# Kernel optimization log

Measured on AMD Instinct MI355X. Metric: run time of the kernel, lower is better.

## Reference

```python
import jax, jax.numpy as jnp
import numpy as np

EMB = 64
L = 2
NU = 100000
NI = 50000
ER = 1000000
ET = 800000
EP = 200000


def setup_inputs() -> dict:
    key = jax.random.key(0)
    ks = jax.random.split(key, 32)
    f = jnp.float32
    def nrm(k, shape, s=0.01):
        return (jax.random.normal(k, shape) * s).astype(f)
    inp = {}
    # graph structure (int)
    inp['rate_src'] = jax.random.randint(ks[0], (ER,), 0, NU)
    inp['rate_dst'] = jax.random.randint(ks[1], (ER,), 0, NI)
    inp['trust_src'] = jax.random.randint(ks[2], (ET,), 0, NU)
    inp['trust_dst'] = jax.random.randint(ks[3], (ET,), 0, NU)
    inp['pos_u'] = jax.random.randint(ks[4], (EP,), 0, NU)
    inp['pos_i'] = jax.random.randint(ks[5], (EP,), 0, NI)
    inp['neg_u'] = jax.random.randint(ks[6], (EP,), 0, NU)
    inp['neg_i'] = jax.random.randint(ks[7], (EP,), 0, NI)
    # embeddings (init normal(0, 0.01) per init_weights)
    inp['eu'] = nrm(ks[8], (NU, EMB))
    inp['ei'] = nrm(ks[9], (NI, EMB))
    # per-rel GATv2 params, stacked over L layers; [:,0]=fc_src, [:,1]=fc_dst
    inp['rate_W'] = nrm(ks[10], (L, 2, EMB, EMB))
    inp['rate_b'] = jnp.zeros((L, 2, EMB), f)
    inp['rate_attn'] = nrm(ks[11], (L, EMB), 0.1)
    inp['rate_bias'] = jnp.zeros((L, EMB), f)
    inp['rb_W'] = nrm(ks[12], (L, 2, EMB, EMB))
    inp['rb_b'] = jnp.zeros((L, 2, EMB), f)
    inp['rb_attn'] = nrm(ks[13], (L, EMB), 0.1)
    inp['rb_bias'] = jnp.zeros((L, EMB), f)
    inp['tr_W'] = nrm(ks[14], (L, 2, EMB, EMB))
    inp['tr_b'] = jnp.zeros((L, 2, EMB), f)
    inp['tr_attn'] = nrm(ks[15], (L, EMB), 0.1)
    inp['tr_bias'] = jnp.zeros((L, EMB), f)
    # attention-gate MLPs: [:, 0]=influence, [:, 1]=interest
    inp['attW1'] = nrm(ks[16], (L, 2, 2 * EMB, 2 * EMB))
    inp['attb1'] = jnp.zeros((L, 2, 2 * EMB), f)
    inp['attW2'] = nrm(ks[17], (L, 2, 2 * EMB))
    inp['attb2'] = jnp.zeros((L, 2), f)
    return inp


def gatv2(hs, hd, src, dst, Ws, bs, Wd, bd, attn, bias, n_dst):
    # DGL GATv2Conv, num_heads=1: e = attn . leaky_relu(Ws h_u + Wd h_v), slope 0.2
    fs = hs @ Ws + bs          # [Ns, E]
    fd = hd @ Wd + bd          # [Nd, E]
    e = jax.nn.leaky_relu(fs[src] + fd[dst], 0.2) @ attn  # [E]
    m = jax.ops.segment_max(e, dst, num_segments=n_dst)
    ex = jnp.exp(e - m[dst])
    denom = jax.ops.segment_sum(ex, dst, num_segments=n_dst)
    alpha = ex / denom[dst]
    out = jax.ops.segment_sum(alpha[:, None] * fs[src], dst, num_segments=n_dst)
    return out + bias


def _bn1(x):
    # BatchNorm1d(1), training-mode batch stats, affine identity at init
    mu = jnp.mean(x)
    var = jnp.mean((x - mu) ** 2)
    return (x - mu) * jax.lax.rsqrt(var + 1e-5)


def reference(eu, ei, rate_W, rate_b, rate_attn, rate_bias, rb_W, rb_b, rb_attn,
              rb_bias, tr_W, tr_b, tr_attn, tr_bias, attW1, attb1, attW2, attb2,
              rate_src, rate_dst, trust_src, trust_dst, pos_u, pos_i, neg_u, neg_i):
    n_users, n_items = eu.shape[0], ei.shape[0]
    hu, hi = eu, ei
    res_u, res_i = [eu], [ei]
    for l in range(rate_W.shape[0]):
        # interest diffusion: rate (user->item) and rated-by (item->user, reverse edges)
        hi_new = gatv2(hu, hi, rate_src, rate_dst, rate_W[l, 0], rate_b[l, 0],
                       rate_W[l, 1], rate_b[l, 1], rate_attn[l], rate_bias[l], n_items) + hi
        q = gatv2(hi, hu, rate_dst, rate_src, rb_W[l, 0], rb_b[l, 0],
                  rb_W[l, 1], rb_b[l, 1], rb_attn[l], rb_bias[l], n_users)
        # influence diffusion: trust (user->user)
        p = gatv2(hu, hu, trust_src, trust_dst, tr_W[l, 0], tr_b[l, 0],
                  tr_W[l, 1], tr_b[l, 1], tr_attn[l], tr_bias[l], n_users)
        def att(h2, i):
            z = (h2 @ attW1[l, i] + attb1[l, i]) @ attW2[l, i] + attb2[l, i]  # [N]
            return jax.nn.leaky_relu(_bn1(z), 0.01)
        a_inf = att(jnp.concatenate([hu, p], axis=1), 0)
        a_int = att(jnp.concatenate([hu, q], axis=1), 1)
        gamma = jax.nn.softmax(jnp.stack([a_inf, a_int], axis=1), axis=1)  # [N,2]
        hu = gamma[:, 0:1] * p + gamma[:, 1:2] * q + hu
        hi = hi_new
        res_u.append(hu)
        res_i.append(hi)
    hu_all = jnp.concatenate(res_u, axis=1)  # [NU, EMB*(1+L)]
    hi_all = jnp.concatenate(res_i, axis=1)
    pos = jnp.sum(hu_all[pos_u] * hi_all[pos_i], axis=1, keepdims=True)  # [EP,1]
    neg = jnp.sum(hu_all[neg_u] * hi_all[neg_i], axis=1, keepdims=True)
    return pos, neg
```

## Files before the change

### kernel.cpp

```cpp
#include <hip/hip_runtime.h>
#include <hip/hip_bf16.h>
#include <hip/hip_fp16.h>
#include <cstdint>

typedef __hip_bfloat16 bf16;
typedef __attribute__((ext_vector_type(8))) short frag_ab;
typedef __attribute__((ext_vector_type(4))) float frag_cd;
typedef __attribute__((ext_vector_type(4))) short short4v;
typedef __attribute__((ext_vector_type(8))) short short8v;
typedef unsigned short u16;

#define CAPA 56
#define CAPB 40
#define CAPC 32

__device__ __forceinline__ float b2f(short s){
  return __uint_as_float(((unsigned)(unsigned short)s) << 16);
}
__device__ __forceinline__ float h2f(short s){
  __half h; __builtin_memcpy(&h, &s, 2); return __half2float(h);
}
__device__ __forceinline__ short f2h_s(float x){
  __half h = __float2half(x);
  short s; __builtin_memcpy(&s, &h, 2); return s;
}
__device__ __forceinline__ void bf_split(float x, short& hi, short& lo){
  bf16 h = __float2bfloat16(x);
  float hf = __bfloat162float(h);
  bf16 l = __float2bfloat16(x - hf);
  __builtin_memcpy(&hi, &h, 2);
  __builtin_memcpy(&lo, &l, 2);
}

__device__ __forceinline__ float wave_sum(float v){
#pragma unroll
  for (int o = 32; o > 0; o >>= 1) v += __shfl_down(v, o, 64);
  return v;
}

__global__ void k_wsplit(const float* __restrict__ rateW, const float* __restrict__ rbW,
                         const float* __restrict__ trW,
                         short* __restrict__ Whi, short* __restrict__ Wlo){
  int tid = blockIdx.x * 256 + threadIdx.x;
  if (tid >= 12 * 4096) return;
  int m = tid >> 12, rem = tid & 4095;
  int lane = rem >> 6, rem2 = rem & 63;
  int pair = rem2 >> 3, j = rem2 & 7;
  int c = pair >> 1, h = pair & 1;
  int rel = m >> 2, li = m & 3;
  const float* base = (rel == 0) ? rateW : (rel == 1) ? rbW : trW;
  float v = base[(size_t)li * 4096 + (32 * h + (lane >> 4) * 8 + j) * 64 + 16 * c + (lane & 15)];
  short sh, sl; bf_split(v, sh, sl);
  Whi[tid] = sh; Wlo[tid] = sl;
}

__device__ __forceinline__ void dev_linear(int rowb, int nloc, int gofs, int nglob,
    const float* __restrict__ x, int xs, int xo,
    const short* __restrict__ Whi, const short* __restrict__ Wlo, int mcount,
    int m0, int m1, int m2, int m3,
    const float* b0, const float* b1, const float* b2, const float* b3,
    bf16* o0, bf16* o1, bf16* o2, bf16* o3){
  int lane = threadIdx.x & 63, w = threadIdx.x >> 6;
  int quad = lane >> 4, n16 = lane & 15;
  int rowbase = rowb + w * 16;
  if (rowbase >= nloc) return;
  int lrow = rowbase + n16; if (lrow >= nloc) lrow = nloc - 1;
  const float* xp = x + (size_t)lrow * xs + xo;
  frag_ab ahi[2], alo[2];
#pragma unroll
  for (int h = 0; h < 2; ++h){
    frag_ab vh, vl;
#pragma unroll
    for (int j = 0; j < 8; ++j){
      float xv = xp[32 * h + quad * 8 + j];
      short sh, sl; bf_split(xv, sh, sl);
      vh[j] = sh; vl[j] = sl;
    }
    ahi[h] = vh; alo[h] = vl;
  }
  int ms[4] = {m0, m1, m2, m3};
  const float* bs[4] = {b0, b1, b2, b3};
  bf16* os[4] = {o0, o1, o2, o3};
  for (int i = 0; i < mcount; ++i){
    const frag_ab* Bh = (const frag_ab*)(Whi + (size_t)ms[i] * 4096 + lane * 64);
    const frag_ab* Bl = (const frag_ab*)(Wlo + (size_t)ms[i] * 4096 + lane * 64);
    frag_cd acc[4];
#pragma unroll
    for (int c = 0; c < 4; ++c) acc[c] = frag_cd{0.f, 0.f, 0.f, 0.f};
#pragma unroll
    for (int c = 0; c < 4; ++c)
#pragma unroll
      for (int h = 0; h < 2; ++h){
        frag_ab bh = Bh[c * 2 + h], bl = Bl[c * 2 + h];
        acc[c] = __builtin_amdgcn_mfma_f32_16x16x32_bf16(ahi[h], bh, acc[c], 0, 0, 0);
        acc[c] = __builtin_amdgcn_mfma_f32_16x16x32_bf16(alo[h], bh, acc[c], 0, 0, 0);
        acc[c] = __builtin_amdgcn_mfma_f32_16x16x32_bf16(ahi[h], bl, acc[c], 0, 0, 0);
      }
    const float* bb = bs[i];
    bf16* oo = os[i];
#pragma unroll
    for (int reg = 0; reg < 4; ++reg){
      int r = rowbase + quad * 4 + reg;
      if (r >= nloc || gofs + r >= nglob) continue;
#pragma unroll
      for (int c = 0; c < 4; ++c)
        oo[(size_t)(gofs + r) * 64 + 16 * c + n16] = __float2bfloat16(acc[c][reg] + bb[16 * c + n16]);
    }
  }
}

struct LinArgs {
  int nblk; const float* x; int xs, xo, n, mcount;
  int m0, m1, m2, m3;
  const float *b0, *b1, *b2, *b3;
  bf16 *o0, *o1, *o2, *o3;
};
struct PrepArgs {
  int NBH, ER, ET;
  const int *rate_src, *rate_dst, *trust_dst;
  int *cntA, *cntB, *cntC;
  u16 *posA, *posB, *posC;
  const short *Whi, *Wlo;
  LinArgs LU, LI;
  const float *W1, *b1v, *W2, *b2v;
  float *vvec, *cs;
};

__global__ void k_prep(PrepArgs a){
  int b = blockIdx.x, t = threadIdx.x;
  if (b < a.NBH){
    int k = b * 256 + t;
    if (k < a.ER){
      int d = a.rate_dst[k], s = a.rate_src[k];
      a.posA[k] = (u16)atomicAdd(a.cntA + d, 1);
      a.posB[k] = (u16)atomicAdd(a.cntB + s, 1);
    }
    if (k < a.ET){
      a.posC[k] = (u16)atomicAdd(a.cntC + a.trust_dst[k], 1);
    }
    return;
  }
  b -= a.NBH;
  if (b < a.LU.nblk){
    dev_linear(b * 64, a.LU.n, 0, a.LU.n, a.LU.x, a.LU.xs, a.LU.xo, a.Whi, a.Wlo,
               a.LU.mcount, a.LU.m0, a.LU.m1, a.LU.m2, a.LU.m3,
               a.LU.b0, a.LU.b1, a.LU.b2, a.LU.b3, a.LU.o0, a.LU.o1, a.LU.o2, a.LU.o3);
    return;
  }
  b -= a.LU.nblk;
  if (b < a.LI.nblk){
    dev_linear(b * 64, a.LI.n, 0, a.LI.n, a.LI.x, a.LI.xs, a.LI.xo, a.Whi, a.Wlo,
               a.LI.mcount, a.LI.m0, a.LI.m1, a.LI.m2, a.LI.m3,
               a.LI.b0, a.LI.b1, a.LI.b2, a.LI.b3, a.LI.o0, a.LI.o1, a.LI.o2, a.LI.o3);
    return;
  }
  for (int it = t; it < 512; it += 256){
    int li = it >> 7, r = it & 127;
    float acc = 0.f;
    for (int c = 0; c < 128; ++c)
      acc += a.W1[(size_t)(li * 128 + r) * 128 + c] * a.W2[li * 128 + c];
    a.vvec[li * 128 + r] = acc;
    if (r == 0){
      float cacc = a.b2v[li];
      for (int c = 0; c < 128; ++c)
        cacc += a.b1v[li * 128 + c] * a.W2[li * 128 + c];
      a.cs[li] = cacc;
    }
  }
}

__global__ void k_fill(const int* __restrict__ rs_, const int* __restrict__ rd_,
                       const int* __restrict__ ts_, const int* __restrict__ td_,
                       const u16* __restrict__ posA, const u16* __restrict__ posB,
                       const u16* __restrict__ posC,
                       int* __restrict__ csrA, u16* __restrict__ csrB,
                       int* __restrict__ csrC, int ER, int ET){
  int k = blockIdx.x * 256 + threadIdx.x;
  if (k < ER){
    int s = rs_[k], d = rd_[k];
    int pa = posA[k], pb = posB[k];
    if (pa < CAPA) csrA[(size_t)d * CAPA + pa] = s;
    if (pb < CAPB) csrB[(size_t)s * CAPB + pb] = (u16)d;
  }
  if (k < ET){
    int pc = posC[k];
    if (pc < CAPC) csrC[(size_t)td_[k] * CAPC + pc] = ts_[k];
  }
}

struct GatArgs {
  int nblk, n, of16;
  const int *cnt;
  const int *csr; const u16 *csr16;
  const bf16 *fs, *fd;
  const float *attn, *bias;
  void *out; int os, oo;
  const float *res; int rs, ro;
};

template<int CAP>
__device__ __forceinline__ void dev_gat(int lb, const GatArgs& g){
  int d = lb * 4 + (threadIdx.x >> 6);
  if (d >= g.n) return;
  int lane = threadIdx.x & 63;
  int gg = lane >> 3, l8 = lane & 7;
  int c = g.cnt[d]; if (c > CAP) c = CAP;
  size_t base = (size_t)d * CAP;
  int my_s = 0;
  if (lane < c) my_s = g.csr16 ? (int)g.csr16[base + lane] : g.csr[base + lane];
  short8v dv = *(const short8v*)(g.fd + (size_t)d * 64 + 8 * l8);
  float fdv[8];
#pragma unroll
  for (int j = 0; j < 8; ++j) fdv[j] = b2f(dv[j]);
  float4 a0 = *(const float4*)(g.attn + 8 * l8);
  float4 a1 = *(const float4*)(g.attn + 8 * l8 + 4);
  float a8[8] = {a0.x, a0.y, a0.z, a0.w, a1.x, a1.y, a1.z, a1.w};
  float acc[8];
#pragma unroll
  for (int j = 0; j < 8; ++j) acc[j] = 0.f;
  float den = 0.f;
  short8v s0, s1;
  {
    int e = gg;
    int ss = __shfl(my_s, (e < c) ? e : 0, 64);
    s0 = *(const short8v*)(g.fs + (size_t)ss * 64 + 8 * l8);
  }
  s1 = s0;
  if (8 < c){
    int e = 8 + gg;
    int ss = __shfl(my_s, (e < c) ? e : 8, 64);
    s1 = *(const short8v*)(g.fs + (size_t)ss * 64 + 8 * l8);
  }
  for (int idx = 0; idx < c; idx += 8){
    short8v cur = s0;
    s0 = s1;
    int nn = idx + 16;
    if (nn < c){
      int e = nn + gg;
      int ss = __shfl(my_s, (e < c) ? e : nn, 64);
      s1 = *(const short8v*)(g.fs + (size_t)ss * 64 + 8 * l8);
    }
    bool valid = (idx + gg) < c;
    float f[8];
    float tt = 0.f;
#pragma unroll
    for (int j = 0; j < 8; ++j){
      f[j] = b2f(cur[j]);
      float v = f[j] + fdv[j];
      v = (v > 0.f) ? v : 0.2f * v;
      tt += v * a8[j];
    }
#pragma unroll
    for (int o = 1; o < 8; o <<= 1) tt += __shfl_xor(tt, o, 64);
    float ex = valid ? __expf(tt) : 0.f;
#pragma unroll
    for (int j = 0; j < 8; ++j) acc[j] += ex * f[j];
    den += ex;
  }
#pragma unroll
  for (int o = 8; o < 64; o <<= 1){
#pragma unroll
    for (int j = 0; j < 8; ++j) acc[j] += __shfl_xor(acc[j], o, 64);
    den += __shfl_xor(den, o, 64);
  }
  if (gg == 0){
    float inv = (den > 0.f) ? 1.f / den : 0.f;
    float4 b0 = *(const float4*)(g.bias + 8 * l8);
    float4 b1 = *(const float4*)(g.bias + 8 * l8 + 4);
    float o8[8];
    o8[0] = acc[0] * inv + b0.x; o8[1] = acc[1] * inv + b0.y;
    o8[2] = acc[2] * inv + b0.z; o8[3] = acc[3] * inv + b0.w;
    o8[4] = acc[4] * inv + b1.x; o8[5] = acc[5] * inv + b1.y;
    o8[6] = acc[6] * inv + b1.z; o8[7] = acc[7] * inv + b1.w;
    if (g.res){
      float4 r0 = *(const float4*)(g.res + (size_t)d * g.rs + g.ro + 8 * l8);
      float4 r1 = *(const float4*)(g.res + (size_t)d * g.rs + g.ro + 8 * l8 + 4);
      o8[0] += r0.x; o8[1] += r0.y; o8[2] += r0.z; o8[3] += r0.w;
      o8[4] += r1.x; o8[5] += r1.y; o8[6] += r1.z; o8[7] += r1.w;
    }
    if (g.of16){
      short8v hv;
#pragma unroll
      for (int j = 0; j < 8; ++j) hv[j] = f2h_s(o8[j]);
      *(short8v*)((short*)g.out + (size_t)d * g.os + g.oo + 8 * l8) = hv;
    } else {
      float* op = (float*)g.out + (size_t)d * g.os + g.oo + 8 * l8;
      *(float4*)op = make_float4(o8[0], o8[1], o8[2], o8[3]);
      *(float4*)(op + 4) = make_float4(o8[4], o8[5], o8[6], o8[7]);
    }
  }
}

template<int CA, int CB, int CC>
__global__ void k_gat3(GatArgs A, GatArgs B, GatArgs C){
  int b = blockIdx.x;
  if (b < A.nblk){ dev_gat<CA>(b, A); return; }
  b -= A.nblk;
  if (b < B.nblk){ dev_gat<CB>(b, B); return; }
  b -= B.nblk;
  dev_gat<CC>(b, C);
}

struct GzArgs {
  int nbz, NU, l;
  const float* hptr;
  const float* pf32;
  const __half* pf16;
  const __half* q;
  const float *vvec, *cs;
  float *z1, *z2, *bsums;
  const short *Whi, *Wlo;
  LinArgs LI;
};

__global__ void k_gatez(GzArgs a){
  int b = blockIdx.x;
  if (b < a.LI.nblk){
    dev_linear(b * 64, a.LI.n, 0, a.LI.n, a.LI.x, a.LI.xs, a.LI.xo, a.Whi, a.Wlo,
               a.LI.mcount, a.LI.m0, a.LI.m1, a.LI.m2, a.LI.m3,
               a.LI.b0, a.LI.b1, a.LI.b2, a.LI.b3, a.LI.o0, a.LI.o1, a.LI.o2, a.LI.o3);
    return;
  }
  b -= a.LI.nblk;
  __shared__ float part[4][4];
  int w = threadIdx.x >> 6, j = threadIdx.x & 63;
  int nidx = b * 4 + w;
  float lz1 = 0.f, lz2 = 0.f;
  if (nidx < a.NU){
    const float* v1 = a.vvec + a.l * 256;
    const float* v2 = a.vvec + a.l * 256 + 128;
    float h  = a.hptr[(size_t)nidx * 64 + j];
    float pv = a.pf16 ? h2f(((const short*)a.pf16)[(size_t)nidx * 64 + j])
                      : a.pf32[(size_t)nidx * 64 + j];
    float qv = h2f(((const short*)a.q)[(size_t)nidx * 64 + j]);
    float t1 = wave_sum(h * v1[j] + pv * v1[64 + j]);
    float t2 = wave_sum(h * v2[j] + qv * v2[64 + j]);
    if (j == 0){
      lz1 = t1 + a.cs[a.l * 2 + 0];
      lz2 = t2 + a.cs[a.l * 2 + 1];
      a.z1[nidx] = lz1;
      a.z2[nidx] = lz2;
    }
  }
  if (j == 0){
    part[w][0] = lz1; part[w][1] = lz1 * lz1;
    part[w][2] = lz2; part[w][3] = lz2 * lz2;
  }
  __syncthreads();
  if (threadIdx.x < 4)
    a.bsums[(size_t)b * 4 + threadIdx.x] =
        part[0][threadIdx.x] + part[1][threadIdx.x] +
        part[2][threadIdx.x] + part[3][threadIdx.x];
}

__global__ void k_bn(const float* __restrict__ bsums, int nb,
                     double* __restrict__ gpart, double* __restrict__ sums,
                     int* __restrict__ tick){
  __shared__ double sh[256];
  __shared__ int lastflag;
  int c = threadIdx.x & 3, r0 = blockIdx.x * 64 + (threadIdx.x >> 2);
  double acc = 0.0;
  for (int i = r0; i < nb; i += gridDim.x * 64)
    acc += (double)bsums[(size_t)i * 4 + c];
  sh[threadIdx.x] = acc;
  __syncthreads();
  for (int s = 128; s >= 4; s >>= 1){
    if (threadIdx.x < s) sh[threadIdx.x] += sh[threadIdx.x + s];
    __syncthreads();
  }
  if (threadIdx.x < 4) gpart[(size_t)blockIdx.x * 4 + threadIdx.x] = sh[threadIdx.x];
  __threadfence();
  if (threadIdx.x == 0) lastflag = (atomicAdd(tick, 1) == (int)gridDim.x - 1);
  __syncthreads();
  if (lastflag){
    __threadfence();
    int k0 = threadIdx.x >> 2;
    double a2 = 0.0;
    for (int i = k0; i < (int)gridDim.x; i += 64) a2 += gpart[(size_t)i * 4 + c];
    sh[threadIdx.x] = a2;
    __syncthreads();
    for (int s = 128; s >= 4; s >>= 1){
      if (threadIdx.x < s) sh[threadIdx.x] += sh[threadIdx.x + s];
      __syncthreads();
    }
    if (threadIdx.x < 4) sums[threadIdx.x] = sh[threadIdx.x];
  }
}

struct CmbArgs {
  int l, NU;
  const float* hptr;
  float* p1; __half* hu2; const __half* q;
  const float *z1, *z2; const double* sums;
  int dolin;
  const short *Whi, *Wlo;
  int m0, m1, m2, m3;
  const float *b0, *b1, *b2, *b3;
  bf16 *o0, *o1, *o2, *o3;
};

__global__ void k_combine(CmbArgs a){
  __shared__ float lds[64][65];
  int r0 = blockIdx.x * 64;
  int t = threadIdx.x;
  double invn = 1.0 / (double)a.NU;
  double mu1 = a.sums[0] * invn, mu2 = a.sums[2] * invn;
  float var1 = (float)(a.sums[1] * invn - mu1 * mu1);
  float var2 = (float)(a.sums[3] * invn - mu2 * mu2);
  float rs1 = rsqrtf(var1 + 1e-5f), rs2 = rsqrtf(var2 + 1e-5f);
  int nloc = a.NU - r0; if (nloc > 64) nloc = 64;
#pragma unroll
  for (int s = 0; s < 16; ++s){
    int elem = s * 256 + t;
    int row = elem >> 6, col = elem & 63;
    if (row < nloc){
      int r = r0 + row;
      float a1 = (a.z1[r] - (float)mu1) * rs1;
      float a2 = (a.z2[r] - (float)mu2) * rs2;
      a1 = a1 > 0.f ? a1 : 0.01f * a1;
      a2 = a2 > 0.f ? a2 : 0.01f * a2;
      float mx = fmaxf(a1, a2);
      float e1 = __expf(a1 - mx), e2 = __expf(a2 - mx);
      float inv = 1.f / (e1 + e2);
      float pv = (a.l == 0) ? a.p1[(size_t)r * 64 + col]
                            : h2f(((const short*)a.hu2)[(size_t)r * 64 + col]);
      float qv = h2f(((const short*)a.q)[(size_t)r * 64 + col]);
      float h  = a.hptr[(size_t)r * 64 + col];
      float out = e1 * inv * pv + e2 * inv * qv + h;
      if (a.l == 0){
        a.p1[(size_t)r * 64 + col] = out;
        lds[row][col] = out;
      } else {
        ((short*)a.hu2)[(size_t)r * 64 + col] = f2h_s(out);
      }
    }
  }
  if (!a.dolin) return;
  __syncthreads();
  dev_linear(0, nloc, r0, a.NU, &lds[0][0], 65, 0, a.Whi, a.Wlo, 4,
             a.m0, a.m1, a.m2, a.m3, a.b0, a.b1, a.b2, a.b3,
             a.o0, a.o1, a.o2, a.o3);
}

__global__ void k_score(const int* __restrict__ pu, const int* __restrict__ pi,
                        const int* __restrict__ nu, const int* __restrict__ ni,
                        const float* __restrict__ eu, const float* __restrict__ p1,
                        const __half* __restrict__ hu2,
                        const float* __restrict__ ei, const float* __restrict__ hi1,
                        const __half* __restrict__ hi2,
                        float* __restrict__ out, int EP){
  int gw = blockIdx.x * 4 + (threadIdx.x >> 6);
  int sub = (threadIdx.x >> 4) & 3, l16 = threadIdx.x & 15;
  int k = gw * 4 + sub;
  if (k >= 2 * EP) return;
  int u, i;
  if (k < EP){ u = pu[k]; i = pi[k]; } else { u = nu[k - EP]; i = ni[k - EP]; }
  float4 a0 = *(const float4*)(eu + (size_t)u * 64 + 4 * l16);
  float4 b0 = *(const float4*)(ei + (size_t)i * 64 + 4 * l16);
  float4 a1 = *(const float4*)(p1 + (size_t)u * 64 + 4 * l16);
  float4 b1 = *(const float4*)(hi1 + (size_t)i * 64 + 4 * l16);
  float acc = a0.x * b0.x + a0.y * b0.y + a0.z * b0.z + a0.w * b0.w
            + a1.x * b1.x + a1.y * b1.y + a1.z * b1.z + a1.w * b1.w;
  short4v ha = *(const short4v*)((const short*)hu2 + (size_t)u * 64 + 4 * l16);
  short4v hb = *(const short4v*)((const short*)hi2 + (size_t)i * 64 + 4 * l16);
  acc += h2f(ha[0]) * h2f(hb[0]) + h2f(ha[1]) * h2f(hb[1])
       + h2f(ha[2]) * h2f(hb[2]) + h2f(ha[3]) * h2f(hb[3]);
#pragma unroll
  for (int o = 8; o > 0; o >>= 1) acc += __shfl_xor(acc, o, 64);
  if (l16 == 0) out[k] = acc;
}

extern "C" void kernel_launch(void* const* d_in, const int* in_sizes, int n_in,
                              void* d_out, int out_size, void* d_ws, size_t ws_size,
                              hipStream_t stream) {
  const int*   rate_src  = (const int*)  d_in[0];
  const int*   rate_dst  = (const int*)  d_in[1];
  const int*   trust_src = (const int*)  d_in[2];
  const int*   trust_dst = (const int*)  d_in[3];
  const int*   pos_u     = (const int*)  d_in[4];
  const int*   pos_i     = (const int*)  d_in[5];
  const int*   neg_u     = (const int*)  d_in[6];
  const int*   neg_i     = (const int*)  d_in[7];
  const float* eu        = (const float*)d_in[8];
  const float* ei        = (const float*)d_in[9];
  const float* rate_W    = (const float*)d_in[10];
  const float* rate_b    = (const float*)d_in[11];
  const float* rate_attn = (const float*)d_in[12];
  const float* rate_bias = (const float*)d_in[13];
  const float* rb_W      = (const float*)d_in[14];
  const float* rb_b      = (const float*)d_in[15];
  const float* rb_attn   = (const float*)d_in[16];
  const float* rb_bias   = (const float*)d_in[17];
  const float* tr_W      = (const float*)d_in[18];
  const float* tr_b      = (const float*)d_in[19];
  const float* tr_attn   = (const float*)d_in[20];
  const float* tr_bias   = (const float*)d_in[21];
  const float* attW1     = (const float*)d_in[22];
  const float* attb1     = (const float*)d_in[23];
  const float* attW2     = (const float*)d_in[24];
  const float* attb2     = (const float*)d_in[25];

  const int ER = in_sizes[0];
  const int ET = in_sizes[2];
  const int EP = in_sizes[4];
  const int NU = in_sizes[8] / 64;
  const int NI = in_sizes[9] / 64;
  const int EM = (ER > ET) ? ER : ET;

  float*  wsp    = (float*)d_ws;
  float*  p1     = wsp;
  float*  hi1    = p1 + (size_t)NU * 64;
  __half* hu2    = (__half*)(hi1 + (size_t)NI * 64);
  __half* hi2    = hu2 + (size_t)NU * 64;
  __half* qf     = hi2 + (size_t)NI * 64;
  u16*    posA   = (u16*)qf;
  u16*    posB   = posA + ER;
  u16*    posC   = posB + ER;
  bf16*   fdA    = (bf16*)(qf + (size_t)NU * 64);
  bf16*   fsB    = fdA + (size_t)NI * 64;
  bf16*   tb     = fsB + (size_t)NI * 64;
  bf16*   fsA    = tb;
  bf16*   fdB    = tb + (size_t)NU * 64;
  bf16*   fsC    = tb + (size_t)NU * 128;
  bf16*   fdC    = tb + (size_t)NU * 192;
  float*  z1     = (float*)(tb + (size_t)NU * 256);
  float*  z2     = z1 + NU;
  float*  bsums  = z2 + NU;
  float*  vvec   = bsums + (size_t)(((NU + 3) / 4) * 4);
  float*  cs     = vvec + 512;
  double* sums   = (double*)(((uintptr_t)(cs + 4) + 15) & ~(uintptr_t)15);
  double* gpart  = sums + 4;
  short*  Whi    = (short*)(gpart + 512);
  short*  Wlo    = Whi + 12 * 4096;
  int*    cntA   = (int*)(Wlo + 12 * 4096);
  int*    cntB   = cntA + NI;
  int*    cntC   = cntB + NU;
  int*    tick   = cntC + NU;
  int*    csrA   = tick + 8;
  u16*    csrB   = (u16*)(csrA + (size_t)NI * CAPA);
  int*    csrC   = (int*)(csrB + (size_t)NU * CAPB);

  auto cdiv = [](int a, int b){ return (a + b - 1) / b; };
  const int nbz = cdiv(NU, 4);

  hipMemsetAsync(cntA, 0, (size_t)(NI + 2 * NU + 8) * 4, stream);
  k_wsplit<<<192, 256, 0, stream>>>(rate_W, rb_W, tr_W, Whi, Wlo);

  PrepArgs pa;
  pa.NBH = cdiv(EM, 256);
  pa.ER = ER; pa.ET = ET;
  pa.rate_src = rate_src; pa.rate_dst = rate_dst; pa.trust_dst = trust_dst;
  pa.cntA = cntA; pa.cntB = cntB; pa.cntC = cntC;
  pa.posA = posA; pa.posB = posB; pa.posC = posC;
  pa.Whi = Whi; pa.Wlo = Wlo;
  pa.LU.nblk = cdiv(NU, 64); pa.LU.x = eu; pa.LU.xs = 64; pa.LU.xo = 0;
  pa.LU.n = NU; pa.LU.mcount = 4;
  pa.LU.m0 = 0; pa.LU.m1 = 5; pa.LU.m2 = 8; pa.LU.m3 = 9;
  pa.LU.b0 = rate_b + 0;  pa.LU.b1 = rb_b + 64;
  pa.LU.b2 = tr_b + 0;    pa.LU.b3 = tr_b + 64;
  pa.LU.o0 = fsA; pa.LU.o1 = fdB; pa.LU.o2 = fsC; pa.LU.o3 = fdC;
  pa.LI.nblk = cdiv(NI, 64); pa.LI.x = ei; pa.LI.xs = 64; pa.LI.xo = 0;
  pa.LI.n = NI; pa.LI.mcount = 2;
  pa.LI.m0 = 1; pa.LI.m1 = 4; pa.LI.m2 = 0; pa.LI.m3 = 0;
  pa.LI.b0 = rate_b + 64; pa.LI.b1 = rb_b + 0;
  pa.LI.b2 = nullptr; pa.LI.b3 = nullptr;
  pa.LI.o0 = fdA; pa.LI.o1 = fsB; pa.LI.o2 = nullptr; pa.LI.o3 = nullptr;
  pa.W1 = attW1; pa.b1v = attb1; pa.W2 = attW2; pa.b2v = attb2;
  pa.vvec = vvec; pa.cs = cs;
  k_prep<<<pa.NBH + pa.LU.nblk + pa.LI.nblk + 1, 256, 0, stream>>>(pa);

  k_fill<<<cdiv(EM, 256), 256, 0, stream>>>(rate_src, rate_dst, trust_src, trust_dst,
      posA, posB, posC, csrA, csrB, csrC, ER, ET);

  for (int l = 0; l < 2; ++l){
    GatArgs A, B, C;
    A.nblk = cdiv(NI, 4); A.n = NI;
    A.cnt = cntA; A.csr = csrA; A.csr16 = nullptr; A.fs = fsA; A.fd = fdA;
    A.attn = rate_attn + l * 64; A.bias = rate_bias + l * 64;
    if (l == 0){ A.of16 = 0; A.out = hi1; A.os = 64; A.oo = 0;
                 A.res = ei;  A.rs = 64; A.ro = 0; }
    else       { A.of16 = 1; A.out = hi2; A.os = 64; A.oo = 0;
                 A.res = hi1; A.rs = 64; A.ro = 0; }
    B.nblk = cdiv(NU, 4); B.n = NU; B.of16 = 1;
    B.cnt = cntB; B.csr = nullptr; B.csr16 = csrB; B.fs = fsB; B.fd = fdB;
    B.attn = rb_attn + l * 64; B.bias = rb_bias + l * 64;
    B.out = qf; B.os = 64; B.oo = 0;
    B.res = nullptr; B.rs = 0; B.ro = 0;
    C.nblk = cdiv(NU, 4); C.n = NU;
    C.cnt = cntC; C.csr = csrC; C.csr16 = nullptr; C.fs = fsC; C.fd = fdC;
    C.attn = tr_attn + l * 64; C.bias = tr_bias + l * 64;
    if (l == 0){ C.of16 = 0; C.out = p1;  C.os = 64; C.oo = 0; }
    else       { C.of16 = 1; C.out = hu2; C.os = 64; C.oo = 0; }
    C.res = nullptr; C.rs = 0; C.ro = 0;
    k_gat3<CAPA, CAPB, CAPC><<<A.nblk + B.nblk + C.nblk, 256, 0, stream>>>(A, B, C);

    GzArgs gz;
    gz.nbz = nbz; gz.NU = NU; gz.l = l;
    gz.hptr = (l == 0) ? eu : p1;
    gz.pf32 = p1;
    gz.pf16 = (l == 0) ? (const __half*)nullptr : hu2;
    gz.q = qf;
    gz.vvec = vvec; gz.cs = cs; gz.z1 = z1; gz.z2 = z2; gz.bsums = bsums;
    gz.Whi = Whi; gz.Wlo = Wlo;
    if (l == 0){
      gz.LI.nblk = cdiv(NI, 64); gz.LI.x = hi1; gz.LI.xs = 64; gz.LI.xo = 0;
      gz.LI.n = NI; gz.LI.mcount = 2;
      gz.LI.m0 = 3; gz.LI.m1 = 6; gz.LI.m2 = 0; gz.LI.m3 = 0;
      gz.LI.b0 = rate_b + 192; gz.LI.b1 = rb_b + 128;
      gz.LI.b2 = nullptr; gz.LI.b3 = nullptr;
      gz.LI.o0 = fdA; gz.LI.o1 = fsB; gz.LI.o2 = nullptr; gz.LI.o3 = nullptr;
    } else {
      gz.LI.nblk = 0; gz.LI.x = nullptr; gz.LI.xs = 0; gz.LI.xo = 0;
      gz.LI.n = 0; gz.LI.mcount = 0;
      gz.LI.m0 = gz.LI.m1 = gz.LI.m2 = gz.LI.m3 = 0;
      gz.LI.b0 = gz.LI.b1 = gz.LI.b2 = gz.LI.b3 = nullptr;
      gz.LI.o0 = gz.LI.o1 = gz.LI.o2 = gz.LI.o3 = nullptr;
    }
    k_gatez<<<nbz + gz.LI.nblk, 256, 0, stream>>>(gz);

    k_bn<<<128, 256, 0, stream>>>(bsums, nbz, gpart, sums, tick + l);

    CmbArgs cm;
    cm.l = l; cm.NU = NU;
    cm.hptr = (l == 0) ? eu : p1;
    cm.p1 = p1; cm.hu2 = hu2; cm.q = qf;
    cm.z1 = z1; cm.z2 = z2; cm.sums = sums;
    cm.dolin = (l == 0) ? 1 : 0;
    cm.Whi = Whi; cm.Wlo = Wlo;
    cm.m0 = 2; cm.m1 = 7; cm.m2 = 10; cm.m3 = 11;
    cm.b0 = rate_b + 128; cm.b1 = rb_b + 192;
    cm.b2 = tr_b + 128;   cm.b3 = tr_b + 192;
    cm.o0 = fsA; cm.o1 = fdB; cm.o2 = fsC; cm.o3 = fdC;
    k_combine<<<cdiv(NU, 64), 256, 0, stream>>>(cm);
  }

  k_score<<<cdiv(2 * EP, 16), 256, 0, stream>>>(pos_u, pos_i, neg_u, neg_i,
      eu, p1, hu2, ei, hi1, hi2, (float*)d_out, EP);
}
```

Baseline: 892.7 us.

## Score from fp16 mirrors of embeddings and move tiny setup work to a pre-kernel

Adds fp16 mirror copies of eu, ei, the layer-1 user output p1 and the layer-1 item output hi1, written during preprocessing, the GAT kernel and the combine kernel. The final scoring kernel then gathers only 16-bit rows, with 8 lanes per edge instead of 16, which halves the bytes read per random gather. The weight split and the attention-MLP vector precompute move into a new k_pre kernel, and the slow serial per-thread loop becomes wave reductions. This costs extra writes and conversion passes over all embedding tables, and the fp16 mirrors add rounding error to the scores.

```diff
diff --git a/kernel.cpp b/kernel.cpp
--- a/kernel.cpp
+++ b/kernel.cpp
@@ -38,20 +38,65 @@
   return v;
 }
 
-__global__ void k_wsplit(const float* __restrict__ rateW, const float* __restrict__ rbW,
-                         const float* __restrict__ trW,
-                         short* __restrict__ Whi, short* __restrict__ Wlo){
-  int tid = blockIdx.x * 256 + threadIdx.x;
-  if (tid >= 12 * 4096) return;
-  int m = tid >> 12, rem = tid & 4095;
-  int lane = rem >> 6, rem2 = rem & 63;
-  int pair = rem2 >> 3, j = rem2 & 7;
-  int c = pair >> 1, h = pair & 1;
-  int rel = m >> 2, li = m & 3;
-  const float* base = (rel == 0) ? rateW : (rel == 1) ? rbW : trW;
-  float v = base[(size_t)li * 4096 + (32 * h + (lane >> 4) * 8 + j) * 64 + 16 * c + (lane & 15)];
-  short sh, sl; bf_split(v, sh, sl);
-  Whi[tid] = sh; Wlo[tid] = sl;
+struct PreArgs {
+  int NWS, NCV, NU, NI;
+  const float *rateW, *rbW, *trW;
+  short *Whi, *Wlo;
+  const float *W1, *b1, *W2, *b2;
+  float *vvec, *cs;
+  const float *eu, *ei;
+  __half *euF, *eiF;
+};
+
+__global__ void k_pre(PreArgs a){
+  int b = blockIdx.x, t = threadIdx.x;
+  if (b < a.NWS){
+    int tid = b * 256 + t;
+    int m = tid >> 12, rem = tid & 4095;
+    int lane = rem >> 6, rem2 = rem & 63;
+    int pair = rem2 >> 3, j = rem2 & 7;
+    int c = pair >> 1, h = pair & 1;
+    int rel = m >> 2, li = m & 3;
+    const float* base = (rel == 0) ? a.rateW : (rel == 1) ? a.rbW : a.trW;
+    float v = base[(size_t)li * 4096 + (32 * h + (lane >> 4) * 8 + j) * 64 + 16 * c + (lane & 15)];
+    short sh, sl; bf_split(v, sh, sl);
+    a.Whi[tid] = sh; a.Wlo[tid] = sl;
+    return;
+  }
+  b -= a.NWS;
+  if (b < 128){
+    int w = t >> 6, j = t & 63;
+    int out = b * 4 + w;
+    int li = out >> 7, r = out & 127;
+    float acc = a.W1[(size_t)(li * 128 + r) * 128 + j]      * a.W2[li * 128 + j]
+              + a.W1[(size_t)(li * 128 + r) * 128 + j + 64] * a.W2[li * 128 + j + 64];
+    acc = wave_sum(acc);
+    if (j == 0) a.vvec[out] = acc;
+    return;
+  }
+  b -= 128;
+  if (b < 1){
+    int w = t >> 6, j = t & 63;
+    float acc = a.b1[w * 128 + j]      * a.W2[w * 128 + j]
+              + a.b1[w * 128 + j + 64] * a.W2[w * 128 + j + 64];
+    acc = wave_sum(acc);
+    if (j == 0) a.cs[w] = acc + a.b2[w];
+    return;
+  }
+  b -= 1;
+  int tot = (a.NU + a.NI) * 8;
+  int idx = b * 256 + t;
+  if (idx >= tot) return;
+  int tu = a.NU * 8;
+  const float* src; __half* dst; int g;
+  if (idx < tu){ src = a.eu; dst = a.euF; g = idx; }
+  else { src = a.ei; dst = a.eiF; g = idx - tu; }
+  float4 v0 = *(const float4*)(src + (size_t)g * 8);
+  float4 v1 = *(const float4*)(src + (size_t)g * 8 + 4);
+  short8v h;
+  h[0] = f2h_s(v0.x); h[1] = f2h_s(v0.y); h[2] = f2h_s(v0.z); h[3] = f2h_s(v0.w);
+  h[4] = f2h_s(v1.x); h[5] = f2h_s(v1.y); h[6] = f2h_s(v1.z); h[7] = f2h_s(v1.w);
+  *(short8v*)((short*)dst + (size_t)g * 8) = h;
 }
 
 __device__ __forceinline__ void dev_linear(int rowb, int nloc, int gofs, int nglob,
@@ -122,8 +167,6 @@
   u16 *posA, *posB, *posC;
   const short *Whi, *Wlo;
   LinArgs LU, LI;
-  const float *W1, *b1v, *W2, *b2v;
-  float *vvec, *cs;
 };
 
 __global__ void k_prep(PrepArgs a){
@@ -148,25 +191,9 @@
     return;
   }
   b -= a.LU.nblk;
-  if (b < a.LI.nblk){
-    dev_linear(b * 64, a.LI.n, 0, a.LI.n, a.LI.x, a.LI.xs, a.LI.xo, a.Whi, a.Wlo,
-               a.LI.mcount, a.LI.m0, a.LI.m1, a.LI.m2, a.LI.m3,
-               a.LI.b0, a.LI.b1, a.LI.b2, a.LI.b3, a.LI.o0, a.LI.o1, a.LI.o2, a.LI.o3);
-    return;
-  }
-  for (int it = t; it < 512; it += 256){
-    int li = it >> 7, r = it & 127;
-    float acc = 0.f;
-    for (int c = 0; c < 128; ++c)
-      acc += a.W1[(size_t)(li * 128 + r) * 128 + c] * a.W2[li * 128 + c];
-    a.vvec[li * 128 + r] = acc;
-    if (r == 0){
-      float cacc = a.b2v[li];
-      for (int c = 0; c < 128; ++c)
-        cacc += a.b1v[li * 128 + c] * a.W2[li * 128 + c];
-      a.cs[li] = cacc;
-    }
-  }
+  dev_linear(b * 64, a.LI.n, 0, a.LI.n, a.LI.x, a.LI.xs, a.LI.xo, a.Whi, a.Wlo,
+             a.LI.mcount, a.LI.m0, a.LI.m1, a.LI.m2, a.LI.m3,
+             a.LI.b0, a.LI.b1, a.LI.b2, a.LI.b3, a.LI.o0, a.LI.o1, a.LI.o2, a.LI.o3);
 }
 
 __global__ void k_fill(const int* __restrict__ rs_, const int* __restrict__ rd_,
@@ -196,6 +223,7 @@
   const float *attn, *bias;
   void *out; int os, oo;
   const float *res; int rs, ro;
+  __half *fmir;
 };
 
 template<int CAP>
@@ -287,6 +315,12 @@
       float* op = (float*)g.out + (size_t)d * g.os + g.oo + 8 * l8;
       *(float4*)op = make_float4(o8[0], o8[1], o8[2], o8[3]);
       *(float4*)(op + 4) = make_float4(o8[4], o8[5], o8[6], o8[7]);
+    }
+    if (g.fmir){
+      short8v hv;
+#pragma unroll
+      for (int j = 0; j < 8; ++j) hv[j] = f2h_s(o8[j]);
+      *(short8v*)((short*)g.fmir + (size_t)d * 64 + 8 * l8) = hv;
     }
   }
 }
@@ -391,6 +425,7 @@
   int l, NU;
   const float* hptr;
   float* p1; __half* hu2; const __half* q;
+  __half* p16;
   const float *z1, *z2; const double* sums;
   int dolin;
   const short *Whi, *Wlo;
@@ -430,6 +465,7 @@
       if (a.l == 0){
         a.p1[(size_t)r * 64 + col] = out;
         lds[row][col] = out;
+        if (a.p16) ((short*)a.p16)[(size_t)r * 64 + col] = f2h_s(out);
       } else {
         ((short*)a.hu2)[(size_t)r * 64 + col] = f2h_s(out);
       }
@@ -444,30 +480,30 @@
 
 __global__ void k_score(const int* __restrict__ pu, const int* __restrict__ pi,
                         const int* __restrict__ nu, const int* __restrict__ ni,
-                        const float* __restrict__ eu, const float* __restrict__ p1,
+                        const __half* __restrict__ euF, const __half* __restrict__ p16,
                         const __half* __restrict__ hu2,
-                        const float* __restrict__ ei, const float* __restrict__ hi1,
+                        const __half* __restrict__ eiF, const __half* __restrict__ hi16,
                         const __half* __restrict__ hi2,
                         float* __restrict__ out, int EP){
-  int gw = blockIdx.x * 4 + (threadIdx.x >> 6);
-  int sub = (threadIdx.x >> 4) & 3, l16 = threadIdx.x & 15;
-  int k = gw * 4 + sub;
+  int wv = threadIdx.x >> 6, lane = threadIdx.x & 63;
+  int g = lane >> 3, l8 = lane & 7;
+  int k = (blockIdx.x * 4 + wv) * 8 + g;
   if (k >= 2 * EP) return;
   int u, i;
   if (k < EP){ u = pu[k]; i = pi[k]; } else { u = nu[k - EP]; i = ni[k - EP]; }
-  float4 a0 = *(const float4*)(eu + (size_t)u * 64 + 4 * l16);
-  float4 b0 = *(const float4*)(ei + (size_t)i * 64 + 4 * l16);
-  float4 a1 = *(const float4*)(p1 + (size_t)u * 64 + 4 * l16);
-  float4 b1 = *(const float4*)(hi1 + (size_t)i * 64 + 4 * l16);
-  float acc = a0.x * b0.x + a0.y * b0.y + a0.z * b0.z + a0.w * b0.w
-            + a1.x * b1.x + a1.y * b1.y + a1.z * b1.z + a1.w * b1.w;
-  short4v ha = *(const short4v*)((const short*)hu2 + (size_t)u * 64 + 4 * l16);
-  short4v hb = *(const short4v*)((const short*)hi2 + (size_t)i * 64 + 4 * l16);
-  acc += h2f(ha[0]) * h2f(hb[0]) + h2f(ha[1]) * h2f(hb[1])
-       + h2f(ha[2]) * h2f(hb[2]) + h2f(ha[3]) * h2f(hb[3]);
-#pragma unroll
-  for (int o = 8; o > 0; o >>= 1) acc += __shfl_xor(acc, o, 64);
-  if (l16 == 0) out[k] = acc;
+  short8v a0 = *(const short8v*)((const short*)euF  + (size_t)u * 64 + 8 * l8);
+  short8v b0 = *(const short8v*)((const short*)eiF  + (size_t)i * 64 + 8 * l8);
+  short8v a1 = *(const short8v*)((const short*)p16  + (size_t)u * 64 + 8 * l8);
+  short8v b1 = *(const short8v*)((const short*)hi16 + (size_t)i * 64 + 8 * l8);
+  short8v a2 = *(const short8v*)((const short*)hu2  + (size_t)u * 64 + 8 * l8);
+  short8v b2 = *(const short8v*)((const short*)hi2  + (size_t)i * 64 + 8 * l8);
+  float acc = 0.f;
+#pragma unroll
+  for (int j = 0; j < 8; ++j)
+    acc += h2f(a0[j]) * h2f(b0[j]) + h2f(a1[j]) * h2f(b1[j]) + h2f(a2[j]) * h2f(b2[j]);
+#pragma unroll
+  for (int o = 1; o < 8; o <<= 1) acc += __shfl_xor(acc, o, 64);
+  if (l8 == 0) out[k] = acc;
 }
 
 extern "C" void kernel_launch(void* const* d_in, const int* in_sizes, int n_in,
@@ -539,12 +575,27 @@
   int*    csrA   = tick + 8;
   u16*    csrB   = (u16*)(csrA + (size_t)NI * CAPA);
   int*    csrC   = (int*)(csrB + (size_t)NU * CAPB);
+  uintptr_t fEnd = ((uintptr_t)(csrC + (size_t)NU * CAPC) + 15) & ~(uintptr_t)15;
+  __half* euF  = (__half*)fEnd;
+  __half* eiF  = euF + (size_t)NU * 64;
+  __half* p16  = eiF + (size_t)NI * 64;
+  __half* hi16 = p16 + (size_t)NU * 64;
 
   auto cdiv = [](int a, int b){ return (a + b - 1) / b; };
   const int nbz = cdiv(NU, 4);
 
   hipMemsetAsync(cntA, 0, (size_t)(NI + 2 * NU + 8) * 4, stream);
-  k_wsplit<<<192, 256, 0, stream>>>(rate_W, rb_W, tr_W, Whi, Wlo);
+
+  PreArgs pr;
+  pr.NWS = 192;
+  pr.NCV = cdiv((NU + NI) * 8, 256);
+  pr.NU = NU; pr.NI = NI;
+  pr.rateW = rate_W; pr.rbW = rb_W; pr.trW = tr_W;
+  pr.Whi = Whi; pr.Wlo = Wlo;
+  pr.W1 = attW1; pr.b1 = attb1; pr.W2 = attW2; pr.b2 = attb2;
+  pr.vvec = vvec; pr.cs = cs;
+  pr.eu = eu; pr.ei = ei; pr.euF = euF; pr.eiF = eiF;
+  k_pre<<<pr.NWS + 128 + 1 + pr.NCV, 256, 0, stream>>>(pr);
 
   PrepArgs pa;
   pa.NBH = cdiv(EM, 256);
@@ -565,9 +616,7 @@
   pa.LI.b0 = rate_b + 64; pa.LI.b1 = rb_b + 0;
   pa.LI.b2 = nullptr; pa.LI.b3 = nullptr;
   pa.LI.o0 = fdA; pa.LI.o1 = fsB; pa.LI.o2 = nullptr; pa.LI.o3 = nullptr;
-  pa.W1 = attW1; pa.b1v = attb1; pa.W2 = attW2; pa.b2v = attb2;
-  pa.vvec = vvec; pa.cs = cs;
-  k_prep<<<pa.NBH + pa.LU.nblk + pa.LI.nblk + 1, 256, 0, stream>>>(pa);
+  k_prep<<<pa.NBH + pa.LU.nblk + pa.LI.nblk, 256, 0, stream>>>(pa);
 
   k_fill<<<cdiv(EM, 256), 256, 0, stream>>>(rate_src, rate_dst, trust_src, trust_dst,
       posA, posB, posC, csrA, csrB, csrC, ER, ET);
@@ -578,20 +627,20 @@
     A.cnt = cntA; A.csr = csrA; A.csr16 = nullptr; A.fs = fsA; A.fd = fdA;
     A.attn = rate_attn + l * 64; A.bias = rate_bias + l * 64;
     if (l == 0){ A.of16 = 0; A.out = hi1; A.os = 64; A.oo = 0;
-                 A.res = ei;  A.rs = 64; A.ro = 0; }
+                 A.res = ei;  A.rs = 64; A.ro = 0; A.fmir = hi16; }
     else       { A.of16 = 1; A.out = hi2; A.os = 64; A.oo = 0;
-                 A.res = hi1; A.rs = 64; A.ro = 0; }
+                 A.res = hi1; A.rs = 64; A.ro = 0; A.fmir = nullptr; }
     B.nblk = cdiv(NU, 4); B.n = NU; B.of16 = 1;
     B.cnt = cntB; B.csr = nullptr; B.csr16 = csrB; B.fs = fsB; B.fd = fdB;
     B.attn = rb_attn + l * 64; B.bias = rb_bias + l * 64;
     B.out = qf; B.os = 64; B.oo = 0;
-    B.res = nullptr; B.rs = 0; B.ro = 0;
+    B.res = nullptr; B.rs = 0; B.ro = 0; B.fmir = nullptr;
     C.nblk = cdiv(NU, 4); C.n = NU;
     C.cnt = cntC; C.csr = csrC; C.csr16 = nullptr; C.fs = fsC; C.fd = fdC;
     C.attn = tr_attn + l * 64; C.bias = tr_bias + l * 64;
     if (l == 0){ C.of16 = 0; C.out = p1;  C.os = 64; C.oo = 0; }
     else       { C.of16 = 1; C.out = hu2; C.os = 64; C.oo = 0; }
-    C.res = nullptr; C.rs = 0; C.ro = 0;
+    C.res = nullptr; C.rs = 0; C.ro = 0; C.fmir = nullptr;
     k_gat3<CAPA, CAPB, CAPC><<<A.nblk + B.nblk + C.nblk, 256, 0, stream>>>(A, B, C);
 
     GzArgs gz;
@@ -624,6 +673,7 @@
     cm.l = l; cm.NU = NU;
     cm.hptr = (l == 0) ? eu : p1;
     cm.p1 = p1; cm.hu2 = hu2; cm.q = qf;
+    cm.p16 = (l == 0) ? p16 : (__half*)nullptr;
     cm.z1 = z1; cm.z2 = z2; cm.sums = sums;
     cm.dolin = (l == 0) ? 1 : 0;
     cm.Whi = Whi; cm.Wlo = Wlo;
@@ -634,6 +684,6 @@
     k_combine<<<cdiv(NU, 64), 256, 0, stream>>>(cm);
   }
 
-  k_score<<<cdiv(2 * EP, 16), 256, 0, stream>>>(pos_u, pos_i, neg_u, neg_i,
-      eu, p1, hu2, ei, hi1, hi2, (float*)d_out, EP);
-}
+  k_score<<<cdiv(2 * EP, 32), 256, 0, stream>>>(pos_u, pos_i, neg_u, neg_i,
+      euF, p16, hu2, eiF, hi16, hi2, (float*)d_out, EP);
+}
```

Measured after the change: 893.9 us. About the same (+0.1%).
